# Kernel tuning notes

Hardware: AMD Instinct MI355X
Metric: run time of the kernel (lower is better)

The kernel has to match this reference:

```python
import jax, jax.numpy as jnp
import numpy as np

B, S, H = 16, 1024, 1024
MAX_SIMS = 100
K_FOCUS = 3  # min(3, seq_len)
SIM_OPTIONS = jnp.array([10, 25, 50, 75, 100], dtype=jnp.int32)


def _gelu(x):
    return jax.nn.gelu(x, approximate=False)  # torch nn.GELU default = exact erf


def _mlp(x, W1, b1, W2, b2):
    return _gelu(x @ W1 + b1) @ W2 + b2


def setup_inputs() -> dict:
    key = jax.random.key(0)
    ks = jax.random.split(key, 24)
    sc = 0.02
    d = {
        'hidden_states': jax.random.normal(ks[0], (B, S, H), dtype=jnp.float32),
        'attention_mask': jnp.ones((B, S), dtype=jnp.int32),
        # simulation_controller: Linear(H,H) -> GELU -> Linear(H,5)
        'Wsc1': jax.random.normal(ks[1], (H, H)) * sc, 'bsc1': jnp.zeros((H,)),
        'Wsc2': jax.random.normal(ks[2], (H, 5)) * sc, 'bsc2': jnp.zeros((5,)),
        # policy: Linear(H,H) -> GELU -> Linear(H,H)
        'Wp1': jax.random.normal(ks[3], (H, H)) * sc, 'bp1': jnp.zeros((H,)),
        'Wp2': jax.random.normal(ks[4], (H, H)) * sc, 'bp2': jnp.zeros((H,)),
        # transition: Linear(2H,H) -> GELU -> (Dropout eval=identity) -> Linear(H,H)
        'Wt1': jax.random.normal(ks[5], (2 * H, H)) * sc, 'bt1': jnp.zeros((H,)),
        'Wt2': jax.random.normal(ks[6], (H, H)) * sc, 'bt2': jnp.zeros((H,)),
        # action_value: Linear(2H,H) -> GELU -> Linear(H,1)
        'Wav1': jax.random.normal(ks[7], (2 * H, H)) * sc, 'bav1': jnp.zeros((H,)),
        'Wav2': jax.random.normal(ks[8], (H, 1)) * sc, 'bav2': jnp.zeros((1,)),
        # aggregation: Linear(2H,H) -> GELU -> Linear(H,H)
        'Wg1': jax.random.normal(ks[9], (2 * H, H)) * sc, 'bg1': jnp.zeros((H,)),
        'Wg2': jax.random.normal(ks[10], (H, H)) * sc, 'bg2': jnp.zeros((H,)),
    }
    return d


def reference(hidden_states, attention_mask,
              Wsc1, bsc1, Wsc2, bsc2,
              Wp1, bp1, Wp2, bp2,
              Wt1, bt1, Wt2, bt2,
              Wav1, bav1, Wav2, bav2,
              Wg1, bg1, Wg2, bg2):
    b, s, h = hidden_states.shape
    root = hidden_states
    # eval-mode sim count selection: argmax over controller logits
    sim_logits = _mlp(root[:, 0], Wsc1, bsc1, Wsc2, bsc2)          # [B,5]
    sims = SIM_OPTIONS[jnp.argmax(sim_logits, axis=-1)]            # [B]

    policy_scores = _mlp(root, Wp1, bp1, Wp2, bp2)                 # [B,S,H]
    focus_logits = policy_scores.mean(axis=-1)                     # [B,S]
    focus_logits = jnp.where(attention_mask == 0, -1e9, focus_logits)
    root_mean = root.mean(axis=1)                                  # [B,H]
    brange = jnp.arange(b)
    base_key = jax.random.key(42)

    def step(acc, t):
        k = jax.random.fold_in(base_key, t)
        # multinomial without replacement via Gumbel top-k on the logits
        g = jax.random.gumbel(k, (b, s), dtype=focus_logits.dtype)
        _, focus_pos = jax.lax.top_k(focus_logits + g, K_FOCUS)    # [B,3]
        focus_states = jnp.take_along_axis(root, focus_pos[:, :, None], axis=1)  # [B,3,H]
        current = root
        for j in range(K_FOCUS):
            trans_in = jnp.concatenate([current.mean(axis=1), focus_states[:, j]], axis=-1)  # [B,2H]
            new_state = _mlp(trans_in, Wt1, bt1, Wt2, bt2)         # [B,H]
            current = current.at[brange, focus_pos[:, j]].set(new_state)
        value = _mlp(jnp.concatenate([root_mean, current.mean(axis=1)], axis=-1),
                     Wav1, bav1, Wav2, bav2)                       # [B,1]
        w = jax.nn.sigmoid(value)[:, :, None]                      # [B,1,1]
        active = (t < sims).astype(current.dtype)[:, None, None]   # mask sims beyond per-example count
        return acc + active * w * current, None

    acc, _ = jax.lax.scan(step, root, jnp.arange(MAX_SIMS))
    enhanced = _mlp(jnp.concatenate([root, acc], axis=-1), Wg1, bg1, Wg2, bg2)
    return hidden_states + enhanced
```

## Files before the change

### kernel.cpp

```cpp
#include <hip/hip_runtime.h>
#include <hip/hip_bf16.h>
#include <cstdint>
#include <math.h>


#define SEQ 1024
#define BATCH 16
#define HDIM 1024
#define NSIM 100
#define NCHAIN (NSIM * BATCH)
#define NCH3 (3 * NCHAIN)
#define SHC (SEQ * HDIM)

typedef short bf16x8 __attribute__((ext_vector_type(8)));
typedef float f32x4 __attribute__((ext_vector_type(4)));
typedef float float4v __attribute__((ext_vector_type(4)));

__device__ __forceinline__ unsigned short f2bf(float f) {
    union { float f; uint32_t u; } c; c.f = f;
    uint32_t u = c.u;
    return (unsigned short)((u + 0x7FFFu + ((u >> 16) & 1u)) >> 16);
}
__device__ __forceinline__ float bf2f(unsigned short h) {
    union { uint32_t u; float f; } c; c.u = ((uint32_t)h) << 16;
    return c.f;
}

__device__ __forceinline__ void gll16(const void* g, void* l) {
    __builtin_amdgcn_global_load_lds(
        (const __attribute__((address_space(1))) void*)g,
        (__attribute__((address_space(3))) void*)l, 16, 0, 0);
}

__device__ __forceinline__ float gelu32(float x) {
    return 0.5f * x * (1.0f + erff(x * 0.70710678f));
}

__device__ __forceinline__ void swz_block(int& bx, int& by) {
    int gx = gridDim.x;
    int h = blockIdx.y * gx + blockIdx.x;
    int nwg = gx * gridDim.y;
    int l = (h & 7) * (nwg >> 3) + (h >> 3);
    bx = l % gx; by = l / gx;
}

__device__ __forceinline__ uint32_t rotl32(uint32_t v, int r) {
    return (v << r) | (v >> (32 - r));
}

__device__ __forceinline__ void threefry(uint32_t k0, uint32_t k1,
                                         uint32_t c0, uint32_t c1,
                                         uint32_t& o0, uint32_t& o1) {
    uint32_t ks0 = k0, ks1 = k1, ks2 = k0 ^ k1 ^ 0x1BD11BDAu;
    uint32_t x0 = c0 + ks0, x1 = c1 + ks1;
#define TFR(r) { x0 += x1; x1 = rotl32(x1, r); x1 ^= x0; }
    TFR(13) TFR(15) TFR(26) TFR(6)   x0 += ks1; x1 += ks2 + 1u;
    TFR(17) TFR(29) TFR(16) TFR(24)  x0 += ks2; x1 += ks0 + 2u;
    TFR(13) TFR(15) TFR(26) TFR(6)   x0 += ks0; x1 += ks1 + 3u;
    TFR(17) TFR(29) TFR(16) TFR(24)  x0 += ks1; x1 += ks2 + 4u;
    TFR(13) TFR(15) TFR(26) TFR(6)   x0 += ks2; x1 += ks0 + 5u;
#undef TFR
    o0 = x0; o1 = x1;
}

__device__ __forceinline__ bool better(float va, int ia, float vb, int ib) {
    return (va > vb) || (va == vb && ia < ib);
}

__global__ __launch_bounds__(256)
void transpose_bf16(const float* __restrict__ W, unsigned short* __restrict__ WT,
                    int K, int N) {
    __shared__ float t[32][33];
    int kb = blockIdx.x * 32, nb = blockIdx.y * 32;
    int tx = threadIdx.x & 31, ty4 = threadIdx.x >> 5;
#pragma unroll
    for (int p = 0; p < 4; ++p) {
        int ky = ty4 + p * 8;
        t[ky][tx] = W[(long)(kb + ky) * N + nb + tx];
    }
    __syncthreads();
#pragma unroll
    for (int p = 0; p < 4; ++p) {
        int ny = ty4 + p * 8;
        WT[(long)(nb + ny) * K + kb + tx] = f2bf(t[tx][ny]);
    }
}

__global__ __launch_bounds__(256)
void transpose_split3(const float* __restrict__ W, unsigned short* __restrict__ WT3,
                      int K, int N) {
    __shared__ float t[32][33];
    int kb = blockIdx.x * 32, nb = blockIdx.y * 32;
    int tx = threadIdx.x & 31, ty4 = threadIdx.x >> 5;
#pragma unroll
    for (int p = 0; p < 4; ++p) {
        int ky = ty4 + p * 8;
        t[ky][tx] = W[(long)(kb + ky) * N + nb + tx];
    }
    __syncthreads();
#pragma unroll
    for (int p = 0; p < 4; ++p) {
        int ny = ty4 + p * 8;
        float w = t[tx][ny];
        unsigned short h = f2bf(w);
        unsigned short l = f2bf(w - bf2f(h));
        long base = (long)(nb + ny) * 3072;
        WT3[base + kb + tx] = h;
        WT3[base + 1024 + kb + tx] = l;
        WT3[base + 2048 + kb + tx] = h;
    }
}

__global__ __launch_bounds__(256)
void cvt_split(const float* __restrict__ src, unsigned short* __restrict__ hi,
               unsigned short* __restrict__ lo, long n8) {
    long i = (long)blockIdx.x * 256 + threadIdx.x;
    long stride = (long)gridDim.x * 256;
    for (; i < n8; i += stride) {
        const float* s = src + i * 8;
        float4v v0 = *(const float4v*)s;
        float4v v1 = *(const float4v*)(s + 4);
        bf16x8 h, l;
#pragma unroll
        for (int e = 0; e < 4; ++e) {
            unsigned short h0 = f2bf(v0[e]);
            h[e] = (short)h0;
            unsigned short h1 = f2bf(v1[e]);
            h[e + 4] = (short)h1;
            if (lo) {
                l[e] = (short)f2bf(v0[e] - bf2f(h0));
                l[e + 4] = (short)f2bf(v1[e] - bf2f(h1));
            }
        }
        *(bf16x8*)&hi[i * 8] = h;
        if (lo) *(bf16x8*)&lo[i * 8] = l;
    }
}

template<int TM, int TN, int BK, int EPI>
__global__ __launch_bounds__(512)
void gemm_bt(const unsigned short* __restrict__ Av1, long lda1, const int* __restrict__ a1rows,
             const unsigned short* __restrict__ Av2, long lda2, const int* __restrict__ a2rows,
             int K1, int kmod1,
             const unsigned short* __restrict__ WT,
             const float* __restrict__ bias,
             const float* __restrict__ wp2m, double* __restrict__ fl64,
             const float* __restrict__ Cadd,
             float* __restrict__ C,
             unsigned short* __restrict__ Cbf,
             long ldc, int M, int N, int K, int doGelu) {
    constexpr int MT = TM / 32;
    constexpr int NT = TN / 64;
    constexpr int WROWS = TM / 2;
    constexpr int WCOLS = TN / 4;
    constexpr int CH = BK / 8;
    constexpr int ASLOT = TM * CH;
    constexpr int BSLOT = TN * CH;
    __shared__ unsigned short As[2][TM * BK];
    __shared__ unsigned short Bs[2][TN * BK];
    __shared__ int r1s[TM], r2s[TM];
    int tid = threadIdx.x;
    int bx, by; swz_block(bx, by);
    int row0 = by * TM, col0 = bx * TN;
    if (tid < TM) {
        int gm = row0 + tid; if (gm >= M) gm = M - 1;
        r1s[tid] = a1rows ? a1rows[gm] : gm;
        r2s[tid] = a2rows ? a2rows[gm] : gm;
    }
    int wid = tid >> 6, lane = tid & 63;
    int wr = wid >> 2, wc = wid & 3;
    int llo = lane & 15, lhi = lane >> 4;
    auto swzc = [](int cs, int r) -> int {
        if constexpr (BK == 64) return cs ^ (r & 7);
        else                    return cs ^ ((r >> 1) & 3);
    };
    f32x4 acc[MT][NT];
#pragma unroll
    for (int i = 0; i < MT; i++)
#pragma unroll
        for (int j = 0; j < NT; j++) acc[i][j] = (f32x4){0.f, 0.f, 0.f, 0.f};
    __syncthreads();

    auto stage = [&](int k0, int b) {
#pragma unroll
        for (int i = 0; i < (BSLOT + 511) / 512; ++i) {
            int q = tid + (i << 9);
            if (BSLOT % 512 == 0 || q < BSLOT) {
                int r = q / CH, cs = q % CH, c = swzc(cs, r);
                gll16(WT + (long)(col0 + r) * K + (k0 + (c << 3)),
                      (char*)Bs[b] + (q << 4));
            }
        }
        bool s1 = (k0 < K1);
        const unsigned short* Ab = s1 ? Av1 : Av2;
        const int* rsel = s1 ? r1s : r2s;
        long lda = s1 ? lda1 : lda2;
        int kb = s1 ? (k0 & kmod1) : (k0 - K1);
#pragma unroll
        for (int i = 0; i < (ASLOT + 511) / 512; ++i) {
            int q = tid + (i << 9);
            if (ASLOT % 512 == 0 || q < ASLOT) {
                int r = q / CH, cs = q % CH, c = swzc(cs, r);
                gll16(Ab + (long)rsel[r] * lda + (kb + (c << 3)),
                      (char*)As[b] + (q << 4));
            }
        }
    };

    stage(0, 0);
    int nIt = K / BK;
    for (int it = 0; it < nIt; ++it) {
        int cur = it & 1;
        __syncthreads();
        if (it + 1 < nIt) stage((it + 1) * BK, cur ^ 1);
        __builtin_amdgcn_sched_barrier(0);
        char* AsB = (char*)As[cur];
        char* BsB = (char*)Bs[cur];
#pragma unroll
        for (int ks = 0; ks < BK / 32; ++ks) {
            bf16x8 af[MT], bfv[NT];
#pragma unroll
            for (int mt = 0; mt < MT; ++mt) {
                int r = wr * WROWS + mt * 16 + llo;
                int pc = swzc((ks << 2) | lhi, r);
                af[mt] = *(const bf16x8*)(AsB + ((r * CH + pc) << 4));
            }
#pragma unroll
            for (int nt = 0; nt < NT; ++nt) {
                int r = wc * WCOLS + nt * 16 + llo;
                int pc = swzc((ks << 2) | lhi, r);
                bfv[nt] = *(const bf16x8*)(BsB + ((r * CH + pc) << 4));
            }
#pragma unroll
            for (int mt = 0; mt < MT; ++mt)
#pragma unroll
                for (int nt = 0; nt < NT; ++nt)
                    acc[mt][nt] = __builtin_amdgcn_mfma_f32_16x16x32_bf16(
                        af[mt], bfv[nt], acc[mt][nt], 0, 0, 0);
        }
    }
    if constexpr (EPI == 0) {
#pragma unroll
        for (int mt = 0; mt < MT; ++mt) {
#pragma unroll
            for (int nt = 0; nt < NT; ++nt) {
                int gn = col0 + wc * WCOLS + nt * 16 + llo;
#pragma unroll
                for (int r = 0; r < 4; ++r) {
                    int gm = row0 + wr * WROWS + mt * 16 + lhi * 4 + r;
                    if (gm >= M) continue;
                    float v = acc[mt][nt][r] + bias[gn];
                    if (doGelu) v = gelu32(v);
                    if (Cadd) v += Cadd[(long)gm * ldc + gn];
                    if (C)   C[(long)gm * ldc + gn] = v;
                    if (Cbf) Cbf[(long)gm * ldc + gn] = f2bf(v);
                }
            }
        }
    } else {
#pragma unroll
        for (int mt = 0; mt < MT; ++mt) {
            double part[4] = {0.0, 0.0, 0.0, 0.0};
#pragma unroll
            for (int nt = 0; nt < NT; ++nt) {
                int gn = col0 + wc * WCOLS + nt * 16 + llo;
                float b = bias[gn], wn = wp2m[gn];
#pragma unroll
                for (int r = 0; r < 4; ++r) {
                    float x = acc[mt][nt][r] + b;
                    part[r] += (double)gelu32(x) * (double)wn;
                }
            }
#pragma unroll
            for (int r = 0; r < 4; ++r) {
                double v = part[r];
                v += __shfl_xor(v, 1);
                v += __shfl_xor(v, 2);
                v += __shfl_xor(v, 4);
                v += __shfl_xor(v, 8);
                if (llo == 0)
                    atomicAdd(&fl64[row0 + wr * WROWS + mt * 16 + lhi * 4 + r], v);
            }
        }
    }
}

__global__ void flbuild_kernel(const double* __restrict__ fl64,
                               const float* __restrict__ wp2m,
                               const int* __restrict__ amask,
                               float* __restrict__ fl32) {
    int m = blockIdx.x * 256 + threadIdx.x;
    fl32[m] = (amask[m] == 0) ? -1e9f : (float)(fl64[m] + (double)wp2m[1024]);
}

__global__ void wp2mean_kernel(const float* __restrict__ Wp2,
                               const float* __restrict__ bp2,
                               float* __restrict__ outv) {
    __shared__ double sb[256];
    int r = blockIdx.x, tid = threadIdx.x;
    const float* src = (r < 1024) ? (Wp2 + (size_t)r * 1024) : bp2;
    double s = 0.0;
    for (int k = tid; k < 1024; k += 256) s += (double)src[k];
    sb[tid] = s; __syncthreads();
    for (int off = 128; off > 0; off >>= 1) {
        if (tid < off) sb[tid] += sb[tid + off];
        __syncthreads();
    }
    if (tid == 0) outv[r] = (float)(sb[0] * (1.0 / 1024.0));
}

__global__ void rootmean_kernel(const float* __restrict__ root, float* __restrict__ rmean,
                                unsigned short* __restrict__ rmean_bf) {
    int b = blockIdx.x;
    int h = blockIdx.y * 256 + threadIdx.x;
    const float* base = root + (size_t)b * SHC + h;
    double s = 0.0;
    for (int ss = 0; ss < SEQ; ss++) s += (double)base[(size_t)ss * HDIM];
    float v = (float)(s * (1.0 / 1024.0));
    rmean[b * HDIM + h] = v;
    rmean_bf[b * HDIM + h] = f2bf(v);
}

__global__ __launch_bounds__(256)
void ctrl_fc1(const float* __restrict__ root, const float* __restrict__ W,
              const float* __restrict__ b1, float* __restrict__ T1) {
    __shared__ double red[16][17];
    int ni = threadIdx.x & 15, kt = threadIdx.x >> 4;
    int n = blockIdx.x * 16 + ni;
    double accb[16];
#pragma unroll
    for (int bb = 0; bb < 16; ++bb) accb[bb] = 0.0;
    for (int k = kt * 64; k < kt * 64 + 64; ++k) {
        double w = (double)W[(long)k * 1024 + n];
#pragma unroll
        for (int bb = 0; bb < 16; ++bb)
            accb[bb] = fma((double)root[(long)bb * SHC + k], w, accb[bb]);
    }
    for (int bb = 0; bb < 16; ++bb) {
        red[kt][ni] = accb[bb];
        __syncthreads();
        if (kt == 0) {
            double s = 0.0;
            for (int q = 0; q < 16; ++q) s += red[q][ni];
            double x = s + (double)b1[n];
            T1[bb * 1024 + n] = (float)(0.5 * x * (1.0 + erf(x * 0.70710678118654752440)));
        }
        __syncthreads();
    }
}

__global__ void ctrl_fc2(const float* __restrict__ T1, const float* __restrict__ W2,
                         const float* __restrict__ b2, float* __restrict__ logits) {
    __shared__ double sb[256];
    int bn = blockIdx.x;
    int b = bn / 5, n = bn % 5;
    double s = 0.0;
    for (int k = threadIdx.x; k < 1024; k += 256)
        s += (double)T1[b * 1024 + k] * (double)W2[k * 5 + n];
    sb[threadIdx.x] = s; __syncthreads();
    for (int off = 128; off > 0; off >>= 1) {
        if (threadIdx.x < off) sb[threadIdx.x] += sb[threadIdx.x + off];
        __syncthreads();
    }
    if (threadIdx.x == 0) logits[b * 5 + n] = (float)(sb[0] + (double)b2[n]);
}

__global__ void sims_kernel(const float* __restrict__ logits, int* __restrict__ sims) {
    int b = threadIdx.x;
    if (b >= BATCH) return;
    float best = logits[b * 5 + 0]; int biv = 0;
    for (int i = 1; i < 5; i++) {
        float v = logits[b * 5 + i];
        if (v > best) { best = v; biv = i; }
    }
    const int opt[5] = {10, 25, 50, 75, 100};
    sims[b] = opt[biv];
}

__global__ void gumbel_kernel(const float* __restrict__ fl,
                              int* __restrict__ idxj, int* __restrict__ vidx) {
    __shared__ float sv[256][3];
    __shared__ int   si[256][3];
    int blk = blockIdx.x;
    int t = blk >> 4, b = blk & 15;
    uint32_t kk0, kk1;
    threefry(0u, 42u, 0u, (uint32_t)t, kk0, kk1);
    int tid = threadIdx.x;
    float bv[3] = {-INFINITY, -INFINITY, -INFINITY};
    int   bi[3] = {0x7FFFFFFF, 0x7FFFFFFF, 0x7FFFFFFF};
    for (int s = tid; s < SEQ; s += 256) {
        uint32_t m = (uint32_t)(b * SEQ + s);
        uint32_t y0, y1;
        threefry(kk0, kk1, 0u, m, y0, y1);
        uint32_t bits = y0 ^ y1;
        float f = __uint_as_float((bits >> 9) | 0x3F800000u) - 1.0f;
        float u = fmaxf(1.17549435e-38f, f);
        float l1 = (float)log((double)u);
        float l2 = (float)log(-(double)l1);
        float g  = -l2;
        float val = fl[b * SEQ + s] + g;
        if (better(val, s, bv[2], bi[2])) {
            bv[2] = val; bi[2] = s;
            if (better(bv[2], bi[2], bv[1], bi[1])) {
                float tv = bv[1]; int ti = bi[1];
                bv[1] = bv[2]; bi[1] = bi[2]; bv[2] = tv; bi[2] = ti;
            }
            if (better(bv[1], bi[1], bv[0], bi[0])) {
                float tv = bv[0]; int ti = bi[0];
                bv[0] = bv[1]; bi[0] = bi[1]; bv[1] = tv; bi[1] = ti;
            }
        }
    }
    sv[tid][0] = bv[0]; sv[tid][1] = bv[1]; sv[tid][2] = bv[2];
    si[tid][0] = bi[0]; si[tid][1] = bi[1]; si[tid][2] = bi[2];
    __syncthreads();
    for (int off = 128; off > 0; off >>= 1) {
        if (tid < off) {
            float av[3] = {sv[tid][0], sv[tid][1], sv[tid][2]};
            int   ai[3] = {si[tid][0], si[tid][1], si[tid][2]};
            float cv[3] = {sv[tid + off][0], sv[tid + off][1], sv[tid + off][2]};
            int   ci[3] = {si[tid + off][0], si[tid + off][1], si[tid + off][2]};
            float rv[3]; int ri[3]; int pa = 0, pb = 0;
#pragma unroll
            for (int r = 0; r < 3; r++) {
                if (better(av[pa], ai[pa], cv[pb], ci[pb])) { rv[r] = av[pa]; ri[r] = ai[pa]; pa++; }
                else                                        { rv[r] = cv[pb]; ri[r] = ci[pb]; pb++; }
            }
            sv[tid][0] = rv[0]; sv[tid][1] = rv[1]; sv[tid][2] = rv[2];
            si[tid][0] = ri[0]; si[tid][1] = ri[1]; si[tid][2] = ri[2];
        }
        __syncthreads();
    }
    if (tid == 0) {
        idxj[0 * NCHAIN + blk] = b * SEQ + si[0][0];
        idxj[1 * NCHAIN + blk] = b * SEQ + si[0][1];
        idxj[2 * NCHAIN + blk] = b * SEQ + si[0][2];
        vidx[blk] = b;
    }
}

__global__ void vidx3_kernel(int* __restrict__ vidx3) {
    int m = blockIdx.x * 256 + threadIdx.x;
    if (m < NCH3) vidx3[m] = m & 15;
}

__global__ void meanfinal_kernel(const float* __restrict__ rmean,
                                 const float* __restrict__ NS,
                                 const float* __restrict__ root,
                                 const int* __restrict__ idxj,
                                 unsigned short* __restrict__ mc_bf) {
    int e = blockIdx.x * 256 + threadIdx.x;
    int c = e >> 10, hh = e & 1023;
    double m = (double)rmean[(c & 15) * HDIM + hh];
#pragma unroll
    for (int j = 0; j < 3; ++j) {
        int r = idxj[j * NCHAIN + c];
        m += ((double)NS[((long)j * NCHAIN + c) * 1024 + hh] -
              (double)root[(long)r * 1024 + hh]) * (1.0 / 1024.0);
    }
    mc_bf[e] = f2bf((float)m);
}

__global__ void valdot_kernel(const float* __restrict__ HV, const float* __restrict__ Wav2,
                              const float* __restrict__ bav2, float* __restrict__ w) {
    __shared__ double sb[256];
    int c = blockIdx.x, tid = threadIdx.x;
    double s = 0.0;
    for (int k = tid; k < HDIM; k += 256) s += (double)HV[(size_t)c * HDIM + k] * (double)Wav2[k];
    sb[tid] = s; __syncthreads();
    for (int off = 128; off > 0; off >>= 1) {
        if (tid < off) sb[tid] += sb[tid + off];
        __syncthreads();
    }
    if (tid == 0) {
        double v = sb[0] + (double)bav2[0];
        w[c] = (float)(1.0 / (1.0 + exp(-v)));
    }
}

__global__ void wsum_kernel(const float* __restrict__ w, const int* __restrict__ sims,
                            double* __restrict__ Wsum) {
    int b = threadIdx.x;
    if (b >= BATCH) return;
    int sb = sims[b];
    double s = 0.0;
    for (int t = 0; t < sb; t++) s += (double)w[t * BATCH + b];
    Wsum[b] = s;
}

__global__ void accinit_kernel(const float* __restrict__ root, const double* __restrict__ Wsum,
                               float* __restrict__ acc) {
    size_t e = (size_t)blockIdx.x * 256 + threadIdx.x;
    int b = (int)(e >> 20);
    acc[e] = (float)((1.0 + Wsum[b]) * (double)root[e]);
}

__global__ __launch_bounds__(256)
void corrections_atomic(const float* __restrict__ NS, const float* __restrict__ root,
                        const float* __restrict__ w, const int* __restrict__ sims,
                        const int* __restrict__ idxj, float* __restrict__ acc) {
    int blk = blockIdx.x;
    int j = blk / NCHAIN, c = blk % NCHAIN;
    int b = c & 15, t = c >> 4;
    if (t >= sims[b]) return;
    float wv = w[c];
    int row = idxj[j * NCHAIN + c];
    const float* ns = NS + ((long)j * NCHAIN + c) * 1024;
    const float* rt = root + (long)row * 1024;
    float* ac = acc + (long)row * 1024;
    for (int h = threadIdx.x; h < 1024; h += 256)
        atomicAdd(&ac[h], wv * (ns[h] - rt[h]));
}

extern "C" void kernel_launch(void* const* d_in, const int* in_sizes, int n_in,
                              void* d_out, int out_size, void* d_ws, size_t ws_size,
                              hipStream_t stream) {
    (void)in_sizes; (void)n_in; (void)out_size; (void)ws_size;
    const float* root = (const float*)d_in[0];
    const int*   amask = (const int*)d_in[1];
    const float* Wsc1 = (const float*)d_in[2];  const float* bsc1 = (const float*)d_in[3];
    const float* Wsc2 = (const float*)d_in[4];  const float* bsc2 = (const float*)d_in[5];
    const float* Wp1  = (const float*)d_in[6];  const float* bp1  = (const float*)d_in[7];
    const float* Wp2  = (const float*)d_in[8];  const float* bp2  = (const float*)d_in[9];
    const float* Wt1  = (const float*)d_in[10]; const float* bt1  = (const float*)d_in[11];
    const float* Wt2  = (const float*)d_in[12]; const float* bt2  = (const float*)d_in[13];
    const float* Wav1 = (const float*)d_in[14]; const float* bav1 = (const float*)d_in[15];
    const float* Wav2 = (const float*)d_in[16]; const float* bav2 = (const float*)d_in[17];
    const float* Wg1  = (const float*)d_in[18]; const float* bg1  = (const float*)d_in[19];
    const float* Wg2  = (const float*)d_in[20]; const float* bg2  = (const float*)d_in[21];
    float* out = (float*)d_out;

    char* p = (char*)d_ws;
    auto carve = [&](size_t nbytes) -> void* {
        void* r = (void*)p; p += (nbytes + 255) & ~(size_t)255; return r;
    };
    unsigned short* H1big = (unsigned short*)carve((size_t)NCH3 * HDIM * 2);
    float*          Hav   = (float*)carve((size_t)NCHAIN * HDIM * 4);
    float*          NS    = (float*)carve((size_t)3 * NCHAIN * HDIM * 4);
    unsigned short* h_bf  = (unsigned short*)H1big;
    unsigned short* WT3   = (unsigned short*)NS;
    unsigned short* WTt1  = (unsigned short*)carve((size_t)1024 * 2048 * 2);
    unsigned short* WTt2  = (unsigned short*)carve((size_t)1024 * 1024 * 2);
    unsigned short* WTav1 = (unsigned short*)carve((size_t)1024 * 2048 * 2);
    unsigned short* WTg1  = (unsigned short*)carve((size_t)1024 * 2048 * 2);
    unsigned short* WTg2  = (unsigned short*)carve((size_t)1024 * 1024 * 2);
    float*  rmean  = (float*)carve(BATCH * HDIM * 4);
    float*  T1     = (float*)carve(BATCH * HDIM * 4);
    float*  logits = (float*)carve(128 * 4);
    float*  wp2m   = (float*)carve(1040 * 4);
    double* fl64   = (double*)carve((size_t)BATCH * SEQ * 8);
    float*  fl32   = (float*)carve(BATCH * SEQ * 4);
    float*  wbuf   = (float*)carve(NCHAIN * 4);
    double* Wsumd  = (double*)carve(64 * 8);
    int*    sims   = (int*)carve(64 * 4);
    int*    idxj   = (int*)carve(3 * NCHAIN * 4);
    int*    vidx   = (int*)carve(NCHAIN * 4);
    int*    vidx3  = (int*)carve(NCH3 * 4);
    unsigned short* root_bf     = (unsigned short*)carve((size_t)BATCH * SEQ * HDIM * 2);
    unsigned short* acc_bf      = (unsigned short*)carve((size_t)BATCH * SEQ * HDIM * 2);
    unsigned short* root_lo     = acc_bf;
    unsigned short* mean_cur_bf = (unsigned short*)carve((size_t)NCHAIN * HDIM * 2);
    unsigned short* rmean_bf    = (unsigned short*)carve(BATCH * HDIM * 2);

    const long NTOT8 = (long)BATCH * SEQ * HDIM / 8;
    const int  KBIG = 1 << 30, KMA = 0x7FFFFFFF;

    transpose_bf16<<<dim3(2048 / 32, 1024 / 32), 256, 0, stream>>>(Wt1, WTt1, 2048, 1024);
    transpose_bf16<<<dim3(1024 / 32, 1024 / 32), 256, 0, stream>>>(Wt2, WTt2, 1024, 1024);
    transpose_bf16<<<dim3(2048 / 32, 1024 / 32), 256, 0, stream>>>(Wav1, WTav1, 2048, 1024);
    transpose_bf16<<<dim3(2048 / 32, 1024 / 32), 256, 0, stream>>>(Wg1, WTg1, 2048, 1024);
    transpose_bf16<<<dim3(1024 / 32, 1024 / 32), 256, 0, stream>>>(Wg2, WTg2, 1024, 1024);
    transpose_split3<<<dim3(32, 32), 256, 0, stream>>>(Wp1, WT3, 1024, 1024);
    cvt_split<<<2048, 256, 0, stream>>>(root, root_bf, root_lo, NTOT8);
    vidx3_kernel<<<(NCH3 + 255) / 256, 256, 0, stream>>>(vidx3);
    wp2mean_kernel<<<1025, 256, 0, stream>>>(Wp2, bp2, wp2m);
    rootmean_kernel<<<dim3(BATCH, HDIM / 256), 256, 0, stream>>>(root, rmean, rmean_bf);
    ctrl_fc1<<<64, 256, 0, stream>>>(root, Wsc1, bsc1, T1);
    ctrl_fc2<<<80, 256, 0, stream>>>(T1, Wsc2, bsc2, logits);
    sims_kernel<<<1, 64, 0, stream>>>(logits, sims);
    hipMemsetAsync(fl64, 0, (size_t)BATCH * SEQ * 8, stream);
    gemm_bt<128, 256, 32, 1><<<dim3(4, 128), 512, 0, stream>>>(
        root_bf, 1024, nullptr, root_lo, 1024, nullptr, 2048, 1023,
        WT3, bp1, wp2m, fl64, nullptr, nullptr, nullptr, 1024,
        BATCH * SEQ, 1024, 3072, 0);
    flbuild_kernel<<<BATCH * SEQ / 256, 256, 0, stream>>>(fl64, wp2m, amask, fl32);
    gumbel_kernel<<<NCHAIN, 256, 0, stream>>>(fl32, idxj, vidx);
    gemm_bt<64, 128, 64, 0><<<dim3(8, 75), 512, 0, stream>>>(
        rmean_bf, 1024, vidx3, root_bf, 1024, idxj, 1024, KMA,
        WTt1, bt1, nullptr, nullptr, nullptr, nullptr, H1big, 1024,
        NCH3, 1024, 2048, 1);
    gemm_bt<64, 128, 64, 0><<<dim3(8, 75), 512, 0, stream>>>(
        H1big, 1024, nullptr, nullptr, 0, nullptr, KBIG, KMA,
        WTt2, bt2, nullptr, nullptr, nullptr, NS, nullptr,
        1024, NCH3, 1024, 1024, 0);
    meanfinal_kernel<<<NCHAIN * HDIM / 256, 256, 0, stream>>>(
        rmean, NS, root, idxj, mean_cur_bf);
    gemm_bt<64, 128, 64, 0><<<dim3(8, 25), 512, 0, stream>>>(
        rmean_bf, 1024, vidx, mean_cur_bf, 1024, nullptr, 1024, KMA,
        WTav1, bav1, nullptr, nullptr, nullptr, Hav, nullptr, 1024,
        NCHAIN, 1024, 2048, 1);
    valdot_kernel<<<NCHAIN, 256, 0, stream>>>(Hav, Wav2, bav2, wbuf);
    wsum_kernel<<<1, 64, 0, stream>>>(wbuf, sims, Wsumd);
    accinit_kernel<<<(BATCH * SEQ * HDIM) / 256, 256, 0, stream>>>(root, Wsumd, out);
    corrections_atomic<<<3 * NCHAIN, 256, 0, stream>>>(NS, root, wbuf, sims, idxj, out);
    cvt_split<<<2048, 256, 0, stream>>>(out, acc_bf, nullptr, NTOT8);
    gemm_bt<128, 256, 32, 0><<<dim3(4, 128), 512, 0, stream>>>(
        root_bf, 1024, nullptr, acc_bf, 1024, nullptr, 1024, KMA,
        WTg1, bg1, nullptr, nullptr, nullptr, nullptr, h_bf, 1024,
        BATCH * SEQ, 1024, 2048, 1);
    gemm_bt<128, 256, 32, 0><<<dim3(4, 128), 512, 0, stream>>>(
        h_bf, 1024, nullptr, nullptr, 0, nullptr, KBIG, KMA,
        WTg2, bg2, nullptr, nullptr, root, out, nullptr, 1024,
        BATCH * SEQ, 1024, 1024, 0);
}
```

Before: 623.6 us.

## Precompute per-batch root-mean projection to halve K of transition and value GEMMs

The first half of the concatenated input to the transition and action-value first layers is the per-batch root mean, identical across all chains of a batch. Its product with the top half of the weight matrix is now computed once per batch in fp32 (rv2_kernel) and added in the GEMM epilogue through a row-index gather, so those GEMMs run with K=1024 instead of 2048 and transpose only half of each weight. The root-mean reduction is also split into a partial-sum kernel plus a finalize kernel for more parallelism. This adds small extra kernels, atomics and memsets, and changes numerics slightly because that half of the product is now fp32 rather than bf16.

```diff
diff --git a/kernel.cpp b/kernel.cpp
--- a/kernel.cpp
+++ b/kernel.cpp
@@ -137,6 +137,42 @@
     }
 }
 
+__global__ __launch_bounds__(256)
+void rv2_kernel(const float* __restrict__ rmean, const float* __restrict__ W,
+                float* __restrict__ Rv) {
+    int blk = blockIdx.x;
+    int b = blk >> 5, nc = (blk >> 3) & 3, kc = blk & 7;
+    int n = (nc << 8) + threadIdx.x;
+    float s = 0.f;
+    int k0 = kc << 7;
+    for (int k = k0; k < k0 + 128; ++k)
+        s = fmaf(rmean[b * 1024 + k], W[(long)k * 1024 + n], s);
+    atomicAdd(&Rv[b * 1024 + n], s);
+}
+
+__global__ __launch_bounds__(256)
+void rootmean_part(const float* __restrict__ root, double* __restrict__ part) {
+    int b = blockIdx.x >> 4, sc = blockIdx.x & 15;
+#pragma unroll
+    for (int hp = 0; hp < 4; ++hp) {
+        int h = (hp << 8) + threadIdx.x;
+        const float* base = root + (size_t)b * SHC + ((size_t)sc << 16) + h;
+        double s = 0.0;
+        for (int ss = 0; ss < 64; ++ss) s += (double)base[(size_t)ss << 10];
+        part[(((long)b << 4) + sc) * 1024 + h] = s;
+    }
+}
+__global__ void rootmean_fin(const double* __restrict__ part, float* __restrict__ rmean,
+                             unsigned short* __restrict__ rmean_bf) {
+    int e = blockIdx.x * 256 + threadIdx.x;
+    int b = e >> 10, h = e & 1023;
+    double s = 0.0;
+    for (int sc = 0; sc < 16; ++sc) s += part[(((long)b << 4) + sc) * 1024 + h];
+    float v = (float)(s * (1.0 / 1024.0));
+    rmean[e] = v;
+    rmean_bf[e] = f2bf(v);
+}
+
 template<int TM, int TN, int BK, int EPI>
 __global__ __launch_bounds__(512)
 void gemm_bt(const unsigned short* __restrict__ Av1, long lda1, const int* __restrict__ a1rows,
@@ -145,6 +181,7 @@
              const unsigned short* __restrict__ WT,
              const float* __restrict__ bias,
              const float* __restrict__ wp2m, double* __restrict__ fl64,
+             const float* __restrict__ Pre,
              const float* __restrict__ Cadd,
              float* __restrict__ C,
              unsigned short* __restrict__ Cbf,
@@ -247,9 +284,11 @@
                 int gn = col0 + wc * WCOLS + nt * 16 + llo;
 #pragma unroll
                 for (int r = 0; r < 4; ++r) {
-                    int gm = row0 + wr * WROWS + mt * 16 + lhi * 4 + r;
+                    int rl = wr * WROWS + mt * 16 + lhi * 4 + r;
+                    int gm = row0 + rl;
                     if (gm >= M) continue;
                     float v = acc[mt][nt][r] + bias[gn];
+                    if (Pre) v += Pre[(long)r2s[rl] * 1024 + gn];
                     if (doGelu) v = gelu32(v);
                     if (Cadd) v += Cadd[(long)gm * ldc + gn];
                     if (C)   C[(long)gm * ldc + gn] = v;
@@ -307,18 +346,6 @@
         __syncthreads();
     }
     if (tid == 0) outv[r] = (float)(sb[0] * (1.0 / 1024.0));
-}
-
-__global__ void rootmean_kernel(const float* __restrict__ root, float* __restrict__ rmean,
-                                unsigned short* __restrict__ rmean_bf) {
-    int b = blockIdx.x;
-    int h = blockIdx.y * 256 + threadIdx.x;
-    const float* base = root + (size_t)b * SHC + h;
-    double s = 0.0;
-    for (int ss = 0; ss < SEQ; ss++) s += (double)base[(size_t)ss * HDIM];
-    float v = (float)(s * (1.0 / 1024.0));
-    rmean[b * HDIM + h] = v;
-    rmean_bf[b * HDIM + h] = f2bf(v);
 }
 
 __global__ __launch_bounds__(256)
@@ -539,12 +566,15 @@
     float*          NS    = (float*)carve((size_t)3 * NCHAIN * HDIM * 4);
     unsigned short* h_bf  = (unsigned short*)H1big;
     unsigned short* WT3   = (unsigned short*)NS;
-    unsigned short* WTt1  = (unsigned short*)carve((size_t)1024 * 2048 * 2);
+    unsigned short* WTt1  = (unsigned short*)carve((size_t)1024 * 1024 * 2);
     unsigned short* WTt2  = (unsigned short*)carve((size_t)1024 * 1024 * 2);
-    unsigned short* WTav1 = (unsigned short*)carve((size_t)1024 * 2048 * 2);
+    unsigned short* WTav1 = (unsigned short*)carve((size_t)1024 * 1024 * 2);
     unsigned short* WTg1  = (unsigned short*)carve((size_t)1024 * 2048 * 2);
     unsigned short* WTg2  = (unsigned short*)carve((size_t)1024 * 1024 * 2);
     float*  rmean  = (float*)carve(BATCH * HDIM * 4);
+    float*  Rv_t   = (float*)carve(BATCH * HDIM * 4);
+    float*  Rv_av  = (float*)carve(BATCH * HDIM * 4);
+    double* rpart  = (double*)carve((size_t)BATCH * 16 * HDIM * 8);
     float*  T1     = (float*)carve(BATCH * HDIM * 4);
     float*  logits = (float*)carve(128 * 4);
     float*  wp2m   = (float*)carve(1040 * 4);
@@ -565,40 +595,47 @@
     const long NTOT8 = (long)BATCH * SEQ * HDIM / 8;
     const int  KBIG = 1 << 30, KMA = 0x7FFFFFFF;
 
-    transpose_bf16<<<dim3(2048 / 32, 1024 / 32), 256, 0, stream>>>(Wt1, WTt1, 2048, 1024);
+    transpose_bf16<<<dim3(1024 / 32, 1024 / 32), 256, 0, stream>>>(
+        Wt1 + (size_t)1024 * 1024, WTt1, 1024, 1024);
     transpose_bf16<<<dim3(1024 / 32, 1024 / 32), 256, 0, stream>>>(Wt2, WTt2, 1024, 1024);
-    transpose_bf16<<<dim3(2048 / 32, 1024 / 32), 256, 0, stream>>>(Wav1, WTav1, 2048, 1024);
+    transpose_bf16<<<dim3(1024 / 32, 1024 / 32), 256, 0, stream>>>(
+        Wav1 + (size_t)1024 * 1024, WTav1, 1024, 1024);
     transpose_bf16<<<dim3(2048 / 32, 1024 / 32), 256, 0, stream>>>(Wg1, WTg1, 2048, 1024);
     transpose_bf16<<<dim3(1024 / 32, 1024 / 32), 256, 0, stream>>>(Wg2, WTg2, 1024, 1024);
     transpose_split3<<<dim3(32, 32), 256, 0, stream>>>(Wp1, WT3, 1024, 1024);
     cvt_split<<<2048, 256, 0, stream>>>(root, root_bf, root_lo, NTOT8);
     vidx3_kernel<<<(NCH3 + 255) / 256, 256, 0, stream>>>(vidx3);
+    hipMemsetAsync(Rv_t, 0, BATCH * HDIM * 4, stream);
+    hipMemsetAsync(Rv_av, 0, BATCH * HDIM * 4, stream);
     wp2mean_kernel<<<1025, 256, 0, stream>>>(Wp2, bp2, wp2m);
-    rootmean_kernel<<<dim3(BATCH, HDIM / 256), 256, 0, stream>>>(root, rmean, rmean_bf);
+    rootmean_part<<<256, 256, 0, stream>>>(root, rpart);
+    rootmean_fin<<<64, 256, 0, stream>>>(rpart, rmean, rmean_bf);
+    rv2_kernel<<<512, 256, 0, stream>>>(rmean, Wt1, Rv_t);
+    rv2_kernel<<<512, 256, 0, stream>>>(rmean, Wav1, Rv_av);
     ctrl_fc1<<<64, 256, 0, stream>>>(root, Wsc1, bsc1, T1);
     ctrl_fc2<<<80, 256, 0, stream>>>(T1, Wsc2, bsc2, logits);
     sims_kernel<<<1, 64, 0, stream>>>(logits, sims);
     hipMemsetAsync(fl64, 0, (size_t)BATCH * SEQ * 8, stream);
     gemm_bt<128, 256, 32, 1><<<dim3(4, 128), 512, 0, stream>>>(
         root_bf, 1024, nullptr, root_lo, 1024, nullptr, 2048, 1023,
-        WT3, bp1, wp2m, fl64, nullptr, nullptr, nullptr, 1024,
+        WT3, bp1, wp2m, fl64, nullptr, nullptr, nullptr, nullptr, 1024,
         BATCH * SEQ, 1024, 3072, 0);
     flbuild_kernel<<<BATCH * SEQ / 256, 256, 0, stream>>>(fl64, wp2m, amask, fl32);
     gumbel_kernel<<<NCHAIN, 256, 0, stream>>>(fl32, idxj, vidx);
     gemm_bt<64, 128, 64, 0><<<dim3(8, 75), 512, 0, stream>>>(
-        rmean_bf, 1024, vidx3, root_bf, 1024, idxj, 1024, KMA,
-        WTt1, bt1, nullptr, nullptr, nullptr, nullptr, H1big, 1024,
-        NCH3, 1024, 2048, 1);
+        root_bf, 1024, idxj, nullptr, 0, vidx3, KBIG, KMA,
+        WTt1, bt1, nullptr, nullptr, Rv_t, nullptr, nullptr, H1big, 1024,
+        NCH3, 1024, 1024, 1);
     gemm_bt<64, 128, 64, 0><<<dim3(8, 75), 512, 0, stream>>>(
         H1big, 1024, nullptr, nullptr, 0, nullptr, KBIG, KMA,
-        WTt2, bt2, nullptr, nullptr, nullptr, NS, nullptr,
+        WTt2, bt2, nullptr, nullptr, nullptr, nullptr, NS, nullptr,
         1024, NCH3, 1024, 1024, 0);
     meanfinal_kernel<<<NCHAIN * HDIM / 256, 256, 0, stream>>>(
         rmean, NS, root, idxj, mean_cur_bf);
     gemm_bt<64, 128, 64, 0><<<dim3(8, 25), 512, 0, stream>>>(
-        rmean_bf, 1024, vidx, mean_cur_bf, 1024, nullptr, 1024, KMA,
-        WTav1, bav1, nullptr, nullptr, nullptr, Hav, nullptr, 1024,
-        NCHAIN, 1024, 2048, 1);
+        mean_cur_bf, 1024, nullptr, nullptr, 0, vidx, KBIG, KMA,
+        WTav1, bav1, nullptr, nullptr, Rv_av, nullptr, Hav, nullptr, 1024,
+        NCHAIN, 1024, 1024, 1);
     valdot_kernel<<<NCHAIN, 256, 0, stream>>>(Hav, Wav2, bav2, wbuf);
     wsum_kernel<<<1, 64, 0, stream>>>(wbuf, sims, Wsumd);
     accinit_kernel<<<(BATCH * SEQ * HDIM) / 256, 256, 0, stream>>>(root, Wsumd, out);
@@ -606,10 +643,10 @@
     cvt_split<<<2048, 256, 0, stream>>>(out, acc_bf, nullptr, NTOT8);
     gemm_bt<128, 256, 32, 0><<<dim3(4, 128), 512, 0, stream>>>(
         root_bf, 1024, nullptr, acc_bf, 1024, nullptr, 1024, KMA,
-        WTg1, bg1, nullptr, nullptr, nullptr, nullptr, h_bf, 1024,
+        WTg1, bg1, nullptr, nullptr, nullptr, nullptr, nullptr, h_bf, 1024,
         BATCH * SEQ, 1024, 2048, 1);
     gemm_bt<128, 256, 32, 0><<<dim3(4, 128), 512, 0, stream>>>(
         h_bf, 1024, nullptr, nullptr, 0, nullptr, KBIG, KMA,
-        WTg2, bg2, nullptr, nullptr, root, out, nullptr, 1024,
+        WTg2, bg2, nullptr, nullptr, nullptr, root, out, nullptr, 1024,
         BATCH * SEQ, 1024, 1024, 0);
 }
```

After: 614.9 us. Within noise of the previous version (-1.4%).
